# Optimization experiments

Measured on AMD Instinct MI355X. Metric: run time of the kernel, lower is better.

## Reference

```python
import jax, jax.numpy as jnp
import numpy as np

NUM_BANDS = 400
LATENT = 8
NUM_LAYERS = 2
K = 10  # num_selected_bands
FF = 128
EPS = 1e-5


def _xavier(key, shape):
    fan_in, fan_out = shape[-1], shape[-2] if len(shape) >= 2 else shape[-1]
    lim = float(np.sqrt(6.0 / (fan_in + fan_out)))
    return jax.random.uniform(key, shape, jnp.float32, -lim, lim)


def setup_inputs() -> dict:
    key = jax.random.key(0)
    ks = jax.random.split(key, 20)
    B, H, W = 1, 256, 256
    d = {
        "x": jax.random.normal(ks[0], (B, NUM_BANDS, H, W), jnp.float32),
        "x_original": jax.random.normal(ks[1], (B, NUM_BANDS, H, W), jnp.float32),
        "pos": _xavier(ks[2], (1, NUM_BANDS)),
        "band_importance": jnp.zeros((NUM_BANDS,), jnp.float32),
        # per-layer transformer params stacked on a leading layer axis
        "Wv": _xavier(ks[3], (NUM_LAYERS, NUM_BANDS, NUM_BANDS)),
        "bv": jnp.zeros((NUM_LAYERS, NUM_BANDS), jnp.float32),
        "Wo": _xavier(ks[4], (NUM_LAYERS, NUM_BANDS, NUM_BANDS)),
        "bo": jnp.zeros((NUM_LAYERS, NUM_BANDS), jnp.float32),
        "ln1_w": jnp.ones((NUM_LAYERS, NUM_BANDS), jnp.float32),
        "ln1_b": jnp.zeros((NUM_LAYERS, NUM_BANDS), jnp.float32),
        "W1": _xavier(ks[5], (NUM_LAYERS, FF, NUM_BANDS)),
        "b1": jnp.zeros((NUM_LAYERS, FF), jnp.float32),
        "W2": _xavier(ks[6], (NUM_LAYERS, NUM_BANDS, FF)),
        "b2": jnp.zeros((NUM_LAYERS, NUM_BANDS), jnp.float32),
        "ln2_w": jnp.ones((NUM_LAYERS, NUM_BANDS), jnp.float32),
        "ln2_b": jnp.zeros((NUM_LAYERS, NUM_BANDS), jnp.float32),
        # lightweight encoder: K -> LATENT -> LATENT
        "We1": _xavier(ks[7], (LATENT, K)),
        "be1": jnp.zeros((LATENT,), jnp.float32),
        "We2": _xavier(ks[8], (LATENT, LATENT)),
        "be2": jnp.zeros((LATENT,), jnp.float32),
        # decoder: LATENT -> LATENT -> NUM_BANDS
        "Wd1": _xavier(ks[9], (LATENT, LATENT)),
        "bd1": jnp.zeros((LATENT,), jnp.float32),
        "Wd2": _xavier(ks[10], (NUM_BANDS, LATENT)),
        "bd2": jnp.zeros((NUM_BANDS,), jnp.float32),
    }
    return d


def _layer_norm(h, w, b):
    mu = jnp.mean(h, axis=-1, keepdims=True)
    var = jnp.mean(jnp.square(h - mu), axis=-1, keepdims=True)
    return (h - mu) * jax.lax.rsqrt(var + EPS) * w + b


def reference(x, x_original, pos, band_importance, Wv, bv, Wo, bo, ln1_w, ln1_b,
              W1, b1, W2, b2, ln2_w, ln2_b, We1, be1, We2, be2, Wd1, bd1, Wd2, bd2):
    B, C, H, W = x.shape
    # [B,C,H,W] -> [B*H*W, C] tokens; learnable positional encoding over bands
    tok = jnp.transpose(x, (0, 2, 3, 1)).reshape(-1, C) + pos

    # TransformerEncoder (post-norm, relu). Seq-first convention => seq_len=1,
    # so softmax over the single score is 1 and self_attn(x) == out_proj(v_proj(x)).
    h = tok
    for i in range(NUM_LAYERS):
        attn = (h @ Wv[i].T + bv[i]) @ Wo[i].T + bo[i]
        h = _layer_norm(h + attn, ln1_w[i], ln1_b[i])
        ff = jax.nn.relu(h @ W1[i].T + b1[i]) @ W2[i].T + b2[i]
        h = _layer_norm(h + ff, ln2_w[i], ln2_b[i])

    attention_scores = h * jax.nn.sigmoid(band_importance)  # [N, C]
    top_v, top_i = jax.lax.top_k(attention_scores, K)       # sorted desc by value
    order = jnp.argsort(top_i, axis=1)
    sorted_idx = jnp.take_along_axis(top_i, order, axis=1)
    sorted_val = jnp.take_along_axis(top_v, order, axis=1)

    orig = jnp.transpose(x_original, (0, 2, 3, 1)).reshape(-1, C)
    selected_bands1 = jnp.take_along_axis(orig, sorted_idx, axis=1)  # [N, K]
    selected = selected_bands1 * sorted_val

    enc = jax.nn.relu(selected @ We1.T + be1) @ We2.T + be2          # [N, LATENT]
    dec = jax.nn.relu(enc @ Wd1.T + bd1) @ Wd2.T + bd2               # [N, C]
    reconstructed = jnp.transpose(dec.reshape(B, H, W, C), (0, 3, 1, 2))
    return reconstructed, sorted_idx, attention_scores, selected_bands1
```

## Files before the change

### kernel.cpp

```cpp
#include <hip/hip_runtime.h>
#include <hip/hip_bf16.h>
#include <math.h>

#define NBANDS 400
#define NPIX   65536
#define FFW    128
#define KSEL   10
#define TOK    16
#define TOKF   32
#define HS     403
#define FS     131
#define HSF    404
#define FSF    132
#define WPAD   512
#define TAU    1e-3f
#define LISTCAP 16384

typedef double f64x4 __attribute__((ext_vector_type(4)));
typedef float  f32x4 __attribute__((ext_vector_type(4)));
#define MFMA64(a,b,c) __builtin_amdgcn_mfma_f64_16x16x4f64((a),(b),(c),0,0,0)

static constexpr size_t WSB_WVOT = 0;
static constexpr size_t WSB_BVO  = 2560000;
static constexpr size_t WSB_SIG  = 2566400;
static constexpr size_t WSB_W1T  = 2569600;
static constexpr size_t WSB_W2T  = 2979200;
static constexpr size_t WSB_WVP  = 3388800;
static constexpr size_t WSB_W2P  = 5027200;
static constexpr size_t WSB_CNT  = 5551488;
static constexpr size_t WSB_LIST = 5551552;
static constexpr size_t WS_NEED  = 5617088;

static constexpr size_t REC_OFF = 0;
static constexpr size_t IDX_OFF = 26214400;
static constexpr size_t SCO_OFF = IDX_OFF + 655360;
static constexpr size_t SEL_OFF = SCO_OFF + 26214400;
static constexpr int    OUT_EXPECT = 53739520;


__global__ void prep_wvot(const float* __restrict__ Wv, const float* __restrict__ Wo,
                          double* __restrict__ WvoT) {
    int b = blockIdx.x;
    int l = b / 400, j = b - l * 400;
    int k = threadIdx.x;
    if (k >= 400) return;
    const float* wo = Wo + l * 160000 + j * 400;
    const float* wv = Wv + l * 160000;
    double acc = 0.0;
    #pragma unroll 4
    for (int m = 0; m < 400; ++m)
        acc += (double)wo[m] * (double)wv[m * 400 + k];
    WvoT[l * 160000 + k * 400 + j] = acc;
}

__global__ void prep_transpose(const float* __restrict__ W1, const float* __restrict__ W2,
                               float* __restrict__ W1T, float* __restrict__ W2T) {
    int idx = blockIdx.x * blockDim.x + threadIdx.x;
    if (idx < 2 * FFW * NBANDS) {
        int l = idx / (FFW * NBANDS); int r = idx - l * (FFW * NBANDS);
        int jf = r / NBANDS; int k = r - jf * NBANDS;
        W1T[l * FFW * NBANDS + k * FFW + jf] = W1[idx];
        int j = r / FFW; int kf = r - j * FFW;
        W2T[l * FFW * NBANDS + kf * NBANDS + j] = W2[idx];
    }
}

__global__ void prep_padf(const double* __restrict__ WvoT, const float* __restrict__ W2T,
                          float* __restrict__ WvoP, float* __restrict__ W2P) {
    int i = blockIdx.x * blockDim.x + threadIdx.x;
    if (i < 2 * 400 * WPAD) {
        int l = i / (400 * WPAD), r = i % (400 * WPAD), k = r / WPAD, c = r % WPAD;
        WvoP[i] = (c < 400) ? (float)WvoT[(size_t)l * 160000 + (size_t)k * 400 + c] : 0.f;
    }
    if (i < 2 * FFW * WPAD) {
        int l = i / (FFW * WPAD), r = i % (FFW * WPAD), k = r / WPAD, c = r % WPAD;
        W2P[i] = (c < 400) ? W2T[(size_t)l * 51200 + (size_t)k * 400 + c] : 0.f;
    }
}

__global__ void prep_small(const float* __restrict__ Wo, const float* __restrict__ bv,
                           const float* __restrict__ bo, const float* __restrict__ bi,
                           double* __restrict__ bvo, double* __restrict__ sigd) {
    int g = blockIdx.x * blockDim.x + threadIdx.x;
    if (g < 800) {
        int l = g / 400;
        const float* wo = Wo + l * 160000 + (g - l * 400) * 400;
        const float* bb = bv + l * 400;
        double acc = (double)bo[g];
        for (int m = 0; m < 400; ++m) acc += (double)wo[m] * (double)bb[m];
        bvo[g] = acc;
    } else if (g < 1200) {
        int c = g - 800;
        sigd[c] = 1.0 / (1.0 + exp(-(double)bi[c]));
    }
}

__global__ void zero_cnt(int* cnt) { if (threadIdx.x == 0) *cnt = 0; }

__global__ void sentinel_kernel(float* out, float v) {
    out[blockIdx.x * 256 + threadIdx.x] = v;
}


__device__ inline void ln_f32(float* __restrict__ hf, float* __restrict__ redf,
                              const float* __restrict__ w, const float* __restrict__ b, int tid) {
    {
        int t = tid >> 4, q = tid & 15;
        float s = 0.f, ss = 0.f;
        for (int j = q; j < NBANDS; j += 16) {
            float v = hf[t * HSF + j]; s += v; ss += v * v;
        }
        #pragma unroll
        for (int m = 1; m < 16; m <<= 1) {
            s  += __shfl_xor(s, m, 64);
            ss += __shfl_xor(ss, m, 64);
        }
        if (q == 0) { redf[t * 2] = s; redf[t * 2 + 1] = ss; }
    }
    __syncthreads();
    for (int idx = tid; idx < TOKF * NBANDS; idx += 512) {
        int t = idx / NBANDS, j = idx - t * NBANDS;
        float mu  = redf[t * 2] * (1.0f / 400.0f);
        float var = redf[t * 2 + 1] * (1.0f / 400.0f) - mu * mu;
        float rs  = 1.0f / sqrtf(var + 1e-5f);
        hf[t * HSF + j] = (hf[t * HSF + j] - mu) * rs * w[j] + b[j];
    }
    __syncthreads();
}

__global__ __launch_bounds__(512, 4) void hbsm_fast(
    const float* __restrict__ x, const float* __restrict__ xo,
    const float* __restrict__ pos,
    const float* __restrict__ ln1w, const float* __restrict__ ln1b,
    const float* __restrict__ b1,   const float* __restrict__ b2,
    const float* __restrict__ ln2w, const float* __restrict__ ln2b,
    const float* __restrict__ We1,  const float* __restrict__ be1,
    const float* __restrict__ We2,  const float* __restrict__ be2,
    const float* __restrict__ Wd1,  const float* __restrict__ bd1,
    const float* __restrict__ Wd2,  const float* __restrict__ bd2,
    const double* __restrict__ bvo, const double* __restrict__ sigd,
    const float* __restrict__ WvoP, const float* __restrict__ W1Tf,
    const float* __restrict__ W2P,
    int* __restrict__ cnt, int* __restrict__ list,
    float* __restrict__ out)
{
    extern __shared__ char smemc[];
    float* hf    = (float*)smemc;
    float* ff    = (float*)(smemc + 51712);
    float* sigsf = (float*)(smemc + 68608);
    float* redf  = (float*)(smemc + 70208);
    float* lvalf = (float*)(smemc + 70464);
    int*   lidx  = (int*)(smemc + 71872);
    float* d1sf  = (float*)(smemc + 73280);

    const int tid = threadIdx.x;
    const int p0  = blockIdx.x * TOKF;

    for (int i = tid; i < NBANDS; i += 512) sigsf[i] = (float)sigd[i];
    for (int i = tid; i < TOKF * NBANDS; i += 512) {
        int t = i & 31, c = i >> 5;
        float xv = __builtin_nontemporal_load(&x[(size_t)c * NPIX + p0 + t]);
        hf[t * HSF + c] = xv + pos[c];
    }
    __syncthreads();

    const int tg = tid >> 7;
    const int cx = tid & 127;
    const int t0 = tg * 8;
    const int jb = cx * 4;
    const bool cw = (jb < NBANDS);

    for (int l = 0; l < 2; ++l) {
        {
            const float* WT = WvoP + (size_t)l * 400 * WPAD;
            f32x4 acc[8];
            #pragma unroll
            for (int i = 0; i < 8; ++i) acc[i] = (f32x4){0,0,0,0};
            #pragma unroll 2
            for (int k4 = 0; k4 < NBANDS; k4 += 4) {
                f32x4 av[8];
                #pragma unroll
                for (int i = 0; i < 8; ++i)
                    av[i] = *(const f32x4*)&hf[(t0 + i) * HSF + k4];
                #pragma unroll
                for (int kk = 0; kk < 4; ++kk) {
                    f32x4 w = *(const f32x4*)&WT[(size_t)(k4 + kk) * WPAD + jb];
                    #pragma unroll
                    for (int i = 0; i < 8; ++i) acc[i] += av[i][kk] * w;
                }
            }
            __syncthreads();
            if (cw) {
                #pragma unroll
                for (int n = 0; n < 4; ++n) {
                    float bvn = (float)bvo[l * 400 + jb + n];
                    #pragma unroll
                    for (int i = 0; i < 8; ++i)
                        hf[(t0 + i) * HSF + jb + n] += acc[i][n] + bvn;
                }
            }
            __syncthreads();
        }
        ln_f32(hf, redf, ln1w + l * 400, ln1b + l * 400, tid);

        {
            const float* WT = W1Tf + (size_t)l * 51200;
            const int jf = cx;
            float acc1[8];
            #pragma unroll
            for (int i = 0; i < 8; ++i) acc1[i] = 0.f;
            #pragma unroll 2
            for (int k4 = 0; k4 < NBANDS; k4 += 4) {
                f32x4 av[8];
                #pragma unroll
                for (int i = 0; i < 8; ++i)
                    av[i] = *(const f32x4*)&hf[(t0 + i) * HSF + k4];
                #pragma unroll
                for (int kk = 0; kk < 4; ++kk) {
                    float w = WT[(size_t)(k4 + kk) * FFW + jf];
                    #pragma unroll
                    for (int i = 0; i < 8; ++i) acc1[i] += av[i][kk] * w;
                }
            }
            float bias = b1[l * FFW + jf];
            #pragma unroll
            for (int i = 0; i < 8; ++i) {
                float v = acc1[i] + bias;
                ff[(t0 + i) * FSF + jf] = v > 0.f ? v : 0.f;
            }
            __syncthreads();
        }

        {
            const float* WT = W2P + (size_t)l * FFW * WPAD;
            f32x4 acc[8];
            #pragma unroll
            for (int i = 0; i < 8; ++i) acc[i] = (f32x4){0,0,0,0};
            #pragma unroll 2
            for (int k4 = 0; k4 < FFW; k4 += 4) {
                f32x4 av[8];
                #pragma unroll
                for (int i = 0; i < 8; ++i)
                    av[i] = *(const f32x4*)&ff[(t0 + i) * FSF + k4];
                #pragma unroll
                for (int kk = 0; kk < 4; ++kk) {
                    f32x4 w = *(const f32x4*)&WT[(size_t)(k4 + kk) * WPAD + jb];
                    #pragma unroll
                    for (int i = 0; i < 8; ++i) acc[i] += av[i][kk] * w;
                }
            }
            if (cw) {
                #pragma unroll
                for (int n = 0; n < 4; ++n) {
                    float bvn = b2[l * 400 + jb + n];
                    #pragma unroll
                    for (int i = 0; i < 8; ++i)
                        hf[(t0 + i) * HSF + jb + n] += acc[i][n] + bvn;
                }
            }
            __syncthreads();
        }
        ln_f32(hf, redf, ln2w + l * 400, ln2b + l * 400, tid);
    }

    for (int idx = tid; idx < TOKF * NBANDS; idx += 512) {
        int t = idx / NBANDS, c = idx - t * NBANDS;
        __builtin_nontemporal_store(hf[t * HSF + c] * sigsf[c],
                                    &out[SCO_OFF + (size_t)(p0 + t) * NBANDS + c]);
    }

    if (tid < TOKF) {
        int t = tid;
        float* lv = lvalf + t * 11;
        int*   li = lidx + t * 11;
        #pragma unroll
        for (int k = 0; k < 11; ++k) { lv[k] = -3.0e38f; li[k] = 0; }
        for (int c = 0; c < NBANDS; ++c) {
            float v = hf[t * HSF + c] * sigsf[c];
            if (v > lv[10]) {
                int j = 10;
                while (j > 0 && lv[j - 1] < v) {
                    lv[j] = lv[j - 1]; li[j] = li[j - 1]; --j;
                }
                lv[j] = v; li[j] = c;
            }
        }
        float margin = lv[9] - lv[10];
        if (margin < TAU) {
            int slot = atomicAdd(cnt, 1);
            if (slot < LISTCAP) list[slot] = p0 + t;
        }
        for (int a = 1; a < KSEL; ++a) {
            float v = lv[a]; int ci = li[a];
            int bq = a - 1;
            while (bq >= 0 && li[bq] > ci) {
                lv[bq + 1] = lv[bq]; li[bq + 1] = li[bq]; --bq;
            }
            lv[bq + 1] = v; li[bq + 1] = ci;
        }
        float sel[KSEL];
        #pragma unroll
        for (int k = 0; k < KSEL; ++k) {
            int ci = li[k];
            float band = __builtin_nontemporal_load(&xo[(size_t)ci * NPIX + p0 + t]);
            __builtin_nontemporal_store((float)ci, &out[IDX_OFF + (size_t)(p0 + t) * KSEL + k]);
            __builtin_nontemporal_store(band, &out[SEL_OFF + (size_t)(p0 + t) * KSEL + k]);
            sel[k] = band * lv[k];
        }
        float e1[8], e2[8];
        #pragma unroll
        for (int e = 0; e < 8; ++e) {
            float acc = be1[e];
            #pragma unroll
            for (int k = 0; k < KSEL; ++k) acc += sel[k] * We1[e * KSEL + k];
            e1[e] = acc > 0.f ? acc : 0.f;
        }
        #pragma unroll
        for (int e = 0; e < 8; ++e) {
            float acc = be2[e];
            #pragma unroll
            for (int j = 0; j < 8; ++j) acc += e1[j] * We2[e * 8 + j];
            e2[e] = acc;
        }
        #pragma unroll
        for (int e = 0; e < 8; ++e) {
            float acc = bd1[e];
            #pragma unroll
            for (int j = 0; j < 8; ++j) acc += e2[j] * Wd1[e * 8 + j];
            d1sf[t * 9 + e] = acc > 0.f ? acc : 0.f;
        }
    }
    __syncthreads();

    for (int idx = tid; idx < TOKF * NBANDS; idx += 512) {
        int t = idx & 31, c = idx >> 5;
        float acc = bd2[c];
        const float* w = Wd2 + c * 8;
        #pragma unroll
        for (int e = 0; e < 8; ++e) acc += d1sf[t * 9 + e] * w[e];
        __builtin_nontemporal_store(acc, &out[REC_OFF + (size_t)c * NPIX + p0 + t]);
    }
}


__device__ inline void layer_norm_inplace(double* __restrict__ h, double* __restrict__ red,
                                          const float* __restrict__ w, const float* __restrict__ b,
                                          int tid) {
    {
        int t = tid >> 5, q = tid & 31;
        double s = 0.0, ss = 0.0;
        for (int j = q; j < NBANDS; j += 32) {
            double v = h[t * HS + j]; s += v; ss += v * v;
        }
        #pragma unroll
        for (int m = 1; m < 32; m <<= 1) {
            s  += __shfl_xor(s, m, 64);
            ss += __shfl_xor(ss, m, 64);
        }
        if (q == 0) { red[t * 2] = s; red[t * 2 + 1] = ss; }
    }
    __syncthreads();
    for (int idx = tid; idx < TOK * NBANDS; idx += 512) {
        int t = idx / NBANDS, j = idx - t * NBANDS;
        double mu  = red[t * 2] / 400.0;
        double var = red[t * 2 + 1] / 400.0 - mu * mu;
        double rs  = 1.0 / sqrt(var + 1e-5);
        h[t * HS + j] = (h[t * HS + j] - mu) * rs * (double)w[j] + (double)b[j];
    }
    __syncthreads();
}

__global__ __launch_bounds__(512) void hbsm_repair(
    const float* __restrict__ x, const float* __restrict__ xo,
    const float* __restrict__ pos,
    const float* __restrict__ ln1w, const float* __restrict__ ln1b,
    const float* __restrict__ b1,   const float* __restrict__ b2,
    const float* __restrict__ ln2w, const float* __restrict__ ln2b,
    const float* __restrict__ We1,  const float* __restrict__ be1,
    const float* __restrict__ We2,  const float* __restrict__ be2,
    const float* __restrict__ Wd1,  const float* __restrict__ bd1,
    const float* __restrict__ Wd2,  const float* __restrict__ bd2,
    const double* __restrict__ WvoT, const double* __restrict__ bvo,
    const double* __restrict__ sigd,
    const float* __restrict__ W1Tf,  const float* __restrict__ W2Tf,
    const int* __restrict__ cnt, const int* __restrict__ list,
    float* __restrict__ out)
{
    const int n = *cnt;
    if ((int)blockIdx.x * TOK >= n) return;

    extern __shared__ double smem[];
    double* h    = smem;
    double* f    = h + TOK * HS;
    double* red  = f + TOK * FS;
    double* lval = red + 64;
    double* sigs = lval + 160;
    float*  d1s  = (float*)(sigs + 400);
    int*    lidx = (int*)(d1s + 144);
    int*    ptok = (int*)(lidx + 160);

    const int tid  = threadIdx.x;
    const int lane = tid & 63;
    const int wv   = tid >> 6;
    const int rA   = lane & 15;
    const int kq   = lane >> 4;

    if (tid < TOK) {
        int slot = blockIdx.x * TOK + tid;
        ptok[tid] = (slot < n && slot < LISTCAP) ? list[slot] : -1;
    }

    int rowm[4], colm[4];
    {
        f64x4 z = {0.0, 0.0, 0.0, 0.0};
        f64x4 pr = MFMA64(0.25 * (double)rA, 1.0, z);
        f64x4 pc = MFMA64(0.25, (double)rA, z);
        #pragma unroll
        for (int i = 0; i < 4; ++i) {
            rowm[i] = ((int)(pr[i] + 0.5)) & 15;
            colm[i] = ((int)(pc[i] + 0.5)) & 15;
        }
    }

    for (int i = tid; i < NBANDS; i += 512) sigs[i] = sigd[i];
    __syncthreads();
    for (int i = tid; i < TOK * NBANDS; i += 512) {
        int t = i & 15, c = i >> 4;
        int pt = ptok[t];
        h[t * HS + c] = (pt >= 0) ? ((double)x[(size_t)c * NPIX + pt] + (double)pos[c]) : 0.0;
    }
    __syncthreads();

    const double* hA = h + rA * HS;
    const int c0 = wv * 16 + rA, c1 = c0 + 128, c2 = c0 + 256;
    const int ct = 384 + rA;
    const bool xtraA = (wv == 0);
    const bool xtraF = (wv == 4);

    for (int l = 0; l < 2; ++l) {
        {
            const double* WT  = WvoT + l * 160000;
            const double* bb0 = bvo + l * 400;
            f64x4 a0={0,0,0,0}, a1={0,0,0,0}, a2={0,0,0,0}, a3={0,0,0,0};
            #pragma unroll 2
            for (int k0 = 0; k0 < NBANDS; k0 += 4) {
                double av = hA[k0 + kq];
                const double* wrow = WT + (size_t)(k0 + kq) * 400;
                a0 = MFMA64(av, wrow[c0], a0);
                a1 = MFMA64(av, wrow[c1], a1);
                a2 = MFMA64(av, wrow[c2], a2);
                if (xtraA) a3 = MFMA64(av, wrow[ct], a3);
            }
            __syncthreads();
            #pragma unroll
            for (int i = 0; i < 4; ++i) {
                int r  = rowm[i];
                int j0 = wv * 16 + colm[i], j1 = j0 + 128, j2 = j0 + 256;
                h[r * HS + j0] += a0[i] + bb0[j0];
                h[r * HS + j1] += a1[i] + bb0[j1];
                h[r * HS + j2] += a2[i] + bb0[j2];
                if (xtraA) {
                    int jtl = 384 + colm[i];
                    h[r * HS + jtl] += a3[i] + bb0[jtl];
                }
            }
            __syncthreads();
        }
        layer_norm_inplace(h, red, ln1w + l * 400, ln1b + l * 400, tid);

        {
            const float* WT  = W1Tf + (size_t)l * 51200;
            const float* bb1 = b1 + l * FFW;
            const int cf = wv * 16 + rA;
            f64x4 e0 = {0,0,0,0};
            #pragma unroll 2
            for (int k0 = 0; k0 < NBANDS; k0 += 4) {
                double av = hA[k0 + kq];
                double b = (double)WT[(size_t)(k0 + kq) * FFW + cf];
                e0 = MFMA64(av, b, e0);
            }
            #pragma unroll
            for (int i = 0; i < 4; ++i) {
                int r  = rowm[i];
                int jf = wv * 16 + colm[i];
                double v0 = e0[i] + (double)bb1[jf];
                f[r * FS + jf] = v0 > 0.0 ? v0 : 0.0;
            }
            __syncthreads();
        }

        {
            const float* WT  = W2Tf + (size_t)l * 51200;
            const float* bb2 = b2 + l * 400;
            const double* fA = f + rA * FS;
            f64x4 a0={0,0,0,0}, a1={0,0,0,0}, a2={0,0,0,0}, a3={0,0,0,0};
            #pragma unroll 2
            for (int k0 = 0; k0 < FFW; k0 += 4) {
                double av = fA[k0 + kq];
                const float* wrow = WT + (size_t)(k0 + kq) * 400;
                a0 = MFMA64(av, (double)wrow[c0], a0);
                a1 = MFMA64(av, (double)wrow[c1], a1);
                a2 = MFMA64(av, (double)wrow[c2], a2);
                if (xtraF) a3 = MFMA64(av, (double)wrow[ct], a3);
            }
            #pragma unroll
            for (int i = 0; i < 4; ++i) {
                int r  = rowm[i];
                int j0 = wv * 16 + colm[i], j1 = j0 + 128, j2 = j0 + 256;
                h[r * HS + j0] += a0[i] + (double)bb2[j0];
                h[r * HS + j1] += a1[i] + (double)bb2[j1];
                h[r * HS + j2] += a2[i] + (double)bb2[j2];
                if (xtraF) {
                    int jtl = 384 + colm[i];
                    h[r * HS + jtl] += a3[i] + (double)bb2[jtl];
                }
            }
            __syncthreads();
        }
        layer_norm_inplace(h, red, ln2w + l * 400, ln2b + l * 400, tid);
    }

    for (int idx = tid; idx < TOK * NBANDS; idx += 512) {
        int t = idx / NBANDS, c = idx - t * NBANDS;
        if (ptok[t] >= 0)
            out[SCO_OFF + (size_t)ptok[t] * NBANDS + c] = (float)(h[t * HS + c] * sigs[c]);
    }

    if (tid < TOK && ptok[tid] >= 0) {
        int t = tid, pt = ptok[t];
        double* lv = lval + t * KSEL;
        int*    li = lidx + t * KSEL;
        #pragma unroll
        for (int k = 0; k < KSEL; ++k) { lv[k] = -1.0e300; li[k] = 0; }
        for (int c = 0; c < NBANDS; ++c) {
            double v = h[t * HS + c] * sigs[c];
            if (v > lv[KSEL - 1]) {
                int j = KSEL - 1;
                while (j > 0 && lv[j - 1] < v) {
                    lv[j] = lv[j - 1]; li[j] = li[j - 1]; --j;
                }
                lv[j] = v; li[j] = c;
            }
        }
        for (int a = 1; a < KSEL; ++a) {
            double v = lv[a]; int ci = li[a];
            int bq = a - 1;
            while (bq >= 0 && li[bq] > ci) {
                lv[bq + 1] = lv[bq]; li[bq + 1] = li[bq]; --bq;
            }
            lv[bq + 1] = v; li[bq + 1] = ci;
        }
        double sel[KSEL];
        #pragma unroll
        for (int k = 0; k < KSEL; ++k) {
            int ci = li[k];
            float band = xo[(size_t)ci * NPIX + pt];
            out[IDX_OFF + (size_t)pt * KSEL + k] = (float)ci;
            out[SEL_OFF + (size_t)pt * KSEL + k] = band;
            sel[k] = (double)band * lv[k];
        }
        double e1[8], e2[8];
        #pragma unroll
        for (int e = 0; e < 8; ++e) {
            double acc = (double)be1[e];
            #pragma unroll
            for (int k = 0; k < KSEL; ++k) acc += sel[k] * (double)We1[e * KSEL + k];
            e1[e] = acc > 0.0 ? acc : 0.0;
        }
        #pragma unroll
        for (int e = 0; e < 8; ++e) {
            double acc = (double)be2[e];
            #pragma unroll
            for (int j = 0; j < 8; ++j) acc += e1[j] * (double)We2[e * 8 + j];
            e2[e] = acc;
        }
        #pragma unroll
        for (int e = 0; e < 8; ++e) {
            double acc = (double)bd1[e];
            #pragma unroll
            for (int j = 0; j < 8; ++j) acc += e2[j] * (double)Wd1[e * 8 + j];
            d1s[t * 9 + e] = (float)(acc > 0.0 ? acc : 0.0);
        }
    }
    __syncthreads();

    for (int idx = tid; idx < TOK * NBANDS; idx += 512) {
        int t = idx & 15, c = idx >> 4;
        if (ptok[t] < 0) continue;
        double acc = (double)bd2[c];
        const float* w = Wd2 + c * 8;
        #pragma unroll
        for (int e = 0; e < 8; ++e) acc += (double)d1s[t * 9 + e] * (double)w[e];
        out[REC_OFF + (size_t)c * NPIX + ptok[t]] = (float)acc;
    }
}

extern "C" void kernel_launch(void* const* d_in, const int* in_sizes, int n_in,
                              void* d_out, int out_size, void* d_ws, size_t ws_size,
                              hipStream_t stream) {
    if (ws_size < WS_NEED) {
        sentinel_kernel<<<dim3(256), dim3(256), 0, stream>>>((float*)d_out, -777.0f);
        return;
    }
    if (out_size != OUT_EXPECT) {
        sentinel_kernel<<<dim3(1), dim3(1), 0, stream>>>((float*)d_out, 1.0e6f);
        return;
    }
    const float* x    = (const float*)d_in[0];
    const float* xo   = (const float*)d_in[1];
    const float* pos  = (const float*)d_in[2];
    const float* bi   = (const float*)d_in[3];
    const float* Wv   = (const float*)d_in[4];
    const float* bv   = (const float*)d_in[5];
    const float* Wo   = (const float*)d_in[6];
    const float* bo   = (const float*)d_in[7];
    const float* ln1w = (const float*)d_in[8];
    const float* ln1b = (const float*)d_in[9];
    const float* W1   = (const float*)d_in[10];
    const float* b1   = (const float*)d_in[11];
    const float* W2   = (const float*)d_in[12];
    const float* b2   = (const float*)d_in[13];
    const float* ln2w = (const float*)d_in[14];
    const float* ln2b = (const float*)d_in[15];
    const float* We1  = (const float*)d_in[16];
    const float* be1  = (const float*)d_in[17];
    const float* We2  = (const float*)d_in[18];
    const float* be2  = (const float*)d_in[19];
    const float* Wd1  = (const float*)d_in[20];
    const float* bd1  = (const float*)d_in[21];
    const float* Wd2  = (const float*)d_in[22];
    const float* bd2  = (const float*)d_in[23];

    char* wsb = (char*)d_ws;
    double* WvoT = (double*)(wsb + WSB_WVOT);
    double* bvo  = (double*)(wsb + WSB_BVO);
    double* sigd = (double*)(wsb + WSB_SIG);
    float*  W1Tf = (float*)(wsb + WSB_W1T);
    float*  W2Tf = (float*)(wsb + WSB_W2T);
    float*  WvoP = (float*)(wsb + WSB_WVP);
    float*  W2P  = (float*)(wsb + WSB_W2P);
    int*    cnt  = (int*)(wsb + WSB_CNT);
    int*    list = (int*)(wsb + WSB_LIST);

    zero_cnt<<<dim3(1), dim3(64), 0, stream>>>(cnt);
    prep_wvot<<<dim3(800), dim3(512), 0, stream>>>(Wv, Wo, WvoT);
    prep_transpose<<<dim3(400), dim3(256), 0, stream>>>(W1, W2, W1Tf, W2Tf);
    prep_padf<<<dim3(800), dim3(512), 0, stream>>>(WvoT, W2Tf, WvoP, W2P);
    prep_small<<<dim3(5), dim3(256), 0, stream>>>(Wo, bv, bo, bi, bvo, sigd);

    const int smem_fast = 74432;
    hipFuncSetAttribute((const void*)hbsm_fast,
                        hipFuncAttributeMaxDynamicSharedMemorySize, smem_fast);
    hipLaunchKernelGGL(hbsm_fast, dim3(2048), dim3(512), smem_fast, stream,
                       x, xo, pos, ln1w, ln1b, b1, b2, ln2w, ln2b,
                       We1, be1, We2, be2, Wd1, bd1, Wd2, bd2,
                       bvo, sigd, WvoP, W1Tf, W2P, cnt, list, (float*)d_out);

    const int smem_rep = 74624;
    hipFuncSetAttribute((const void*)hbsm_repair,
                        hipFuncAttributeMaxDynamicSharedMemorySize, smem_rep);
    hipLaunchKernelGGL(hbsm_repair, dim3(1024), dim3(512), smem_rep, stream,
                       x, xo, pos, ln1w, ln1b, b1, b2, ln2w, ln2b,
                       We1, be1, We2, be2, Wd1, bd1, Wd2, bd2,
                       WvoT, bvo, sigd, W1Tf, W2Tf, cnt, list, (float*)d_out);
    (void)in_sizes; (void)n_in;
}
```

Baseline: 2.310 ms.

## Retile fp32 band GEMMs to 16 tokens x 2 columns with weight prefetch

Changes the per-thread tile of the Wvo and W2 fp32 GEMMs from 8 tokens x 4 output columns to 16 tokens x 2 columns, spreading 512 threads as 2 token groups x 256 column lanes. Each thread now reads half as much of the weight row per token and prefetches the next four weight rows in registers, trying to hide global-memory latency. The W1 GEMM keeps the old 4x128 mapping through separate local indices. In exchange, each thread loads twice as many activation vectors from shared memory per weight load, and the extra accumulators and prefetch registers may raise register pressure.

```diff
diff --git a/kernel.cpp b/kernel.cpp
--- a/kernel.cpp
+++ b/kernel.cpp
@@ -18,6 +18,7 @@
 
 typedef double f64x4 __attribute__((ext_vector_type(4)));
 typedef float  f32x4 __attribute__((ext_vector_type(4)));
+typedef float  f32x2 __attribute__((ext_vector_type(2)));
 #define MFMA64(a,b,c) __builtin_amdgcn_mfma_f64_16x16x4f64((a),(b),(c),0,0,0)
 
 static constexpr size_t WSB_WVOT = 0;
@@ -164,98 +165,142 @@
     }
     __syncthreads();
 
-    const int tg = tid >> 7;
-    const int cx = tid & 127;
-    const int t0 = tg * 8;
-    const int jb = cx * 4;
+    const int tg = tid >> 8;
+    const int cx = tid & 255;
+    const int t0 = tg * 16;
+    const int jb = cx * 2;
     const bool cw = (jb < NBANDS);
 
     for (int l = 0; l < 2; ++l) {
         {
             const float* WT = WvoP + (size_t)l * 400 * WPAD;
-            f32x4 acc[8];
-            #pragma unroll
-            for (int i = 0; i < 8; ++i) acc[i] = (f32x4){0,0,0,0};
+            float acc0[16], acc1[16];
+            #pragma unroll
+            for (int i = 0; i < 16; ++i) { acc0[i] = 0.f; acc1[i] = 0.f; }
+            f32x2 w0 = *(const f32x2*)&WT[jb];
+            f32x2 w1 = *(const f32x2*)&WT[(size_t)1 * WPAD + jb];
+            f32x2 w2 = *(const f32x2*)&WT[(size_t)2 * WPAD + jb];
+            f32x2 w3 = *(const f32x2*)&WT[(size_t)3 * WPAD + jb];
+            for (int k4 = 0; k4 < NBANDS; k4 += 4) {
+                const int kn = (k4 + 4 < NBANDS) ? k4 + 4 : k4;
+                f32x2 n0 = *(const f32x2*)&WT[(size_t)(kn + 0) * WPAD + jb];
+                f32x2 n1 = *(const f32x2*)&WT[(size_t)(kn + 1) * WPAD + jb];
+                f32x2 n2 = *(const f32x2*)&WT[(size_t)(kn + 2) * WPAD + jb];
+                f32x2 n3 = *(const f32x2*)&WT[(size_t)(kn + 3) * WPAD + jb];
+                {
+                    f32x4 av[8];
+                    #pragma unroll
+                    for (int i = 0; i < 8; ++i)
+                        av[i] = *(const f32x4*)&hf[(t0 + i) * HSF + k4];
+                    #pragma unroll
+                    for (int i = 0; i < 8; ++i) {
+                        acc0[i] += av[i][0] * w0[0] + av[i][1] * w1[0] + av[i][2] * w2[0] + av[i][3] * w3[0];
+                        acc1[i] += av[i][0] * w0[1] + av[i][1] * w1[1] + av[i][2] * w2[1] + av[i][3] * w3[1];
+                    }
+                }
+                {
+                    f32x4 av[8];
+                    #pragma unroll
+                    for (int i = 0; i < 8; ++i)
+                        av[i] = *(const f32x4*)&hf[(t0 + 8 + i) * HSF + k4];
+                    #pragma unroll
+                    for (int i = 0; i < 8; ++i) {
+                        acc0[8 + i] += av[i][0] * w0[0] + av[i][1] * w1[0] + av[i][2] * w2[0] + av[i][3] * w3[0];
+                        acc1[8 + i] += av[i][0] * w0[1] + av[i][1] * w1[1] + av[i][2] * w2[1] + av[i][3] * w3[1];
+                    }
+                }
+                w0 = n0; w1 = n1; w2 = n2; w3 = n3;
+            }
+            __syncthreads();
+            if (cw) {
+                float bv0 = (float)bvo[l * 400 + jb];
+                float bv1 = (float)bvo[l * 400 + jb + 1];
+                #pragma unroll
+                for (int i = 0; i < 16; ++i) {
+                    hf[(t0 + i) * HSF + jb]     += acc0[i] + bv0;
+                    hf[(t0 + i) * HSF + jb + 1] += acc1[i] + bv1;
+                }
+            }
+            __syncthreads();
+        }
+        ln_f32(hf, redf, ln1w + l * 400, ln1b + l * 400, tid);
+
+        {
+            const float* WT = W1Tf + (size_t)l * 51200;
+            const int tg4 = tid >> 7;
+            const int jf  = tid & 127;
+            const int t0f = tg4 * 8;
+            float acc1f[8];
+            #pragma unroll
+            for (int i = 0; i < 8; ++i) acc1f[i] = 0.f;
             #pragma unroll 2
             for (int k4 = 0; k4 < NBANDS; k4 += 4) {
                 f32x4 av[8];
                 #pragma unroll
                 for (int i = 0; i < 8; ++i)
-                    av[i] = *(const f32x4*)&hf[(t0 + i) * HSF + k4];
-                #pragma unroll
-                for (int kk = 0; kk < 4; ++kk) {
-                    f32x4 w = *(const f32x4*)&WT[(size_t)(k4 + kk) * WPAD + jb];
-                    #pragma unroll
-                    for (int i = 0; i < 8; ++i) acc[i] += av[i][kk] * w;
-                }
-            }
-            __syncthreads();
-            if (cw) {
-                #pragma unroll
-                for (int n = 0; n < 4; ++n) {
-                    float bvn = (float)bvo[l * 400 + jb + n];
-                    #pragma unroll
-                    for (int i = 0; i < 8; ++i)
-                        hf[(t0 + i) * HSF + jb + n] += acc[i][n] + bvn;
-                }
-            }
-            __syncthreads();
-        }
-        ln_f32(hf, redf, ln1w + l * 400, ln1b + l * 400, tid);
-
-        {
-            const float* WT = W1Tf + (size_t)l * 51200;
-            const int jf = cx;
-            float acc1[8];
-            #pragma unroll
-            for (int i = 0; i < 8; ++i) acc1[i] = 0.f;
-            #pragma unroll 2
-            for (int k4 = 0; k4 < NBANDS; k4 += 4) {
-                f32x4 av[8];
-                #pragma unroll
-                for (int i = 0; i < 8; ++i)
-                    av[i] = *(const f32x4*)&hf[(t0 + i) * HSF + k4];
+                    av[i] = *(const f32x4*)&hf[(t0f + i) * HSF + k4];
                 #pragma unroll
                 for (int kk = 0; kk < 4; ++kk) {
                     float w = WT[(size_t)(k4 + kk) * FFW + jf];
                     #pragma unroll
-                    for (int i = 0; i < 8; ++i) acc1[i] += av[i][kk] * w;
+                    for (int i = 0; i < 8; ++i) acc1f[i] += av[i][kk] * w;
                 }
             }
             float bias = b1[l * FFW + jf];
             #pragma unroll
             for (int i = 0; i < 8; ++i) {
-                float v = acc1[i] + bias;
-                ff[(t0 + i) * FSF + jf] = v > 0.f ? v : 0.f;
+                float v = acc1f[i] + bias;
+                ff[(t0f + i) * FSF + jf] = v > 0.f ? v : 0.f;
             }
             __syncthreads();
         }
 
         {
             const float* WT = W2P + (size_t)l * FFW * WPAD;
-            f32x4 acc[8];
-            #pragma unroll
-            for (int i = 0; i < 8; ++i) acc[i] = (f32x4){0,0,0,0};
-            #pragma unroll 2
+            float acc0[16], acc1[16];
+            #pragma unroll
+            for (int i = 0; i < 16; ++i) { acc0[i] = 0.f; acc1[i] = 0.f; }
+            f32x2 w0 = *(const f32x2*)&WT[jb];
+            f32x2 w1 = *(const f32x2*)&WT[(size_t)1 * WPAD + jb];
+            f32x2 w2 = *(const f32x2*)&WT[(size_t)2 * WPAD + jb];
+            f32x2 w3 = *(const f32x2*)&WT[(size_t)3 * WPAD + jb];
             for (int k4 = 0; k4 < FFW; k4 += 4) {
-                f32x4 av[8];
+                const int kn = (k4 + 4 < FFW) ? k4 + 4 : k4;
+                f32x2 n0 = *(const f32x2*)&WT[(size_t)(kn + 0) * WPAD + jb];
+                f32x2 n1 = *(const f32x2*)&WT[(size_t)(kn + 1) * WPAD + jb];
+                f32x2 n2 = *(const f32x2*)&WT[(size_t)(kn + 2) * WPAD + jb];
+                f32x2 n3 = *(const f32x2*)&WT[(size_t)(kn + 3) * WPAD + jb];
+                {
+                    f32x4 av[8];
+                    #pragma unroll
+                    for (int i = 0; i < 8; ++i)
+                        av[i] = *(const f32x4*)&ff[(t0 + i) * FSF + k4];
+                    #pragma unroll
+                    for (int i = 0; i < 8; ++i) {
+                        acc0[i] += av[i][0] * w0[0] + av[i][1] * w1[0] + av[i][2] * w2[0] + av[i][3] * w3[0];
+                        acc1[i] += av[i][0] * w0[1] + av[i][1] * w1[1] + av[i][2] * w2[1] + av[i][3] * w3[1];
+                    }
+                }
+                {
+                    f32x4 av[8];
+                    #pragma unroll
+                    for (int i = 0; i < 8; ++i)
+                        av[i] = *(const f32x4*)&ff[(t0 + 8 + i) * FSF + k4];
+                    #pragma unroll
+                    for (int i = 0; i < 8; ++i) {
+                        acc0[8 + i] += av[i][0] * w0[0] + av[i][1] * w1[0] + av[i][2] * w2[0] + av[i][3] * w3[0];
+                        acc1[8 + i] += av[i][0] * w0[1] + av[i][1] * w1[1] + av[i][2] * w2[1] + av[i][3] * w3[1];
+                    }
+                }
+                w0 = n0; w1 = n1; w2 = n2; w3 = n3;
+            }
+            if (cw) {
+                float bv0 = b2[l * 400 + jb];
+                float bv1 = b2[l * 400 + jb + 1];
                 #pragma unroll
-                for (int i = 0; i < 8; ++i)
-                    av[i] = *(const f32x4*)&ff[(t0 + i) * FSF + k4];
-                #pragma unroll
-                for (int kk = 0; kk < 4; ++kk) {
-                    f32x4 w = *(const f32x4*)&WT[(size_t)(k4 + kk) * WPAD + jb];
-                    #pragma unroll
-                    for (int i = 0; i < 8; ++i) acc[i] += av[i][kk] * w;
-                }
-            }
-            if (cw) {
-                #pragma unroll
-                for (int n = 0; n < 4; ++n) {
-                    float bvn = b2[l * 400 + jb + n];
-                    #pragma unroll
-                    for (int i = 0; i < 8; ++i)
-                        hf[(t0 + i) * HSF + jb + n] += acc[i][n] + bvn;
+                for (int i = 0; i < 16; ++i) {
+                    hf[(t0 + i) * HSF + jb]     += acc0[i] + bv0;
+                    hf[(t0 + i) * HSF + jb + 1] += acc1[i] + bv1;
                 }
             }
             __syncthreads();
```

Result: no change. 2.353 ms (+1.9%).
